# Kernel optimization log

Hardware: AMD Instinct MI355X
Metric: run time of the kernel (lower is better)

The kernel has to match this reference:

```python
import jax, jax.numpy as jnp
import numpy as np
from jax import lax

NEG = jnp.float32(-1e9)
POS = jnp.float32(1e9)


def _edt_sq(mask):
    """Exact squared Euclidean distance transform of a 2D boolean mask.

    mask: [H, W] bool, True = foreground (nonzero in scipy terms).
    Returns [H, W] float32 squared distance to nearest background (False) pixel.
    Felzenszwalb-Huttenlocher separable formulation:
      pass 1 (axis 0): 1D distance to nearest zero per column (O(H) via scans)
      pass 2 (axis 1): min-plus convolution with quadratic per row.
    """
    H, W = mask.shape
    zero = ~mask
    idx = jnp.broadcast_to(jnp.arange(H, dtype=jnp.float32)[:, None], (H, W))
    # index of last background pixel at-or-above, and next at-or-below, per column
    last0 = lax.associative_scan(jnp.maximum, jnp.where(zero, idx, NEG), axis=0)
    next0 = jnp.flip(
        lax.associative_scan(jnp.minimum, jnp.flip(jnp.where(zero, idx, POS), 0), axis=0), 0)
    d1 = jnp.minimum(idx - last0, next0 - idx)  # 1D distance along axis 0
    f = jnp.where(mask, d1 * d1, jnp.float32(0.0))  # squared axis-0 distance
    # pass 2: D[i, j] = min_j' f[i, j'] + (j - j')^2
    jq = jnp.arange(W, dtype=jnp.float32)
    q = (jq[:, None] - jq[None, :]) ** 2  # [W, W]
    def row_min(frow):  # frow: [W]
        return jnp.min(frow[None, :] + q, axis=1)  # [W]
    return lax.map(row_min, f)  # [H, W]


def setup_inputs() -> dict:
    key = jax.random.key(0)
    img = jax.random.uniform(key, (2048, 2048), dtype=jnp.float32)
    return {"img": img}


def reference(img) -> jnp.ndarray:
    mask = img > 0.5  # scipy: nonzero pixels are foreground
    d = jnp.sqrt(_edt_sq(mask))
    m = jnp.max(d)
    d = jnp.where(m > 0, d / m * 255.0, d)  # `if img.max() != 0: img = img/max*255`
    return d.astype(jnp.uint8)  # img.astype(np.uint8)
```

## Files before the change

### kernel.cpp

```cpp
#include <hip/hip_runtime.h>
#include <math.h>

typedef unsigned long long u64;

#define H 2048
#define W 2048
#define NWR 64
#define TILE 128
#define HALO 32
#define LW 192
#define LSTRIDE 193
#define DCLAMP 2900
#define NTHR 256

__device__ __attribute__((noinline)) int vfar_up(const unsigned* rmask, int col, int r, int ks) {
    for (int kk = ks - 2; kk >= 0; --kk) {
        unsigned w = rmask[kk * W + col];
        if (w) return r - (kk * 32 + (31 - __clz(w)));
    }
    return DCLAMP;
}
__device__ __attribute__((noinline)) int vfar_dn(const unsigned* rmask, int col, int r, int ks) {
    for (int kk = ks + 2; kk < NWR; ++kk) {
        unsigned w = rmask[kk * W + col];
        if (w) return (kk * 32 + (__ffs(w) - 1)) - r;
    }
    return DCLAMP;
}

__device__ __attribute__((noinline)) float f_from_mask(const unsigned* rmask, int col, int r) {
    int kw = r >> 5, b = r & 31;
    unsigned wm1 = (kw > 0)       ? rmask[(kw - 1) * W + col] : 0u;
    unsigned w0  =                  rmask[kw * W + col];
    unsigned wp1 = (kw < NWR - 1) ? rmask[(kw + 1) * W + col] : 0u;
    if ((w0 >> b) & 1u) return 0.0f;
    u64 A  = (u64)wm1 | ((u64)w0 << 32);
    u64 Bv = (u64)w0  | ((u64)wp1 << 32);
    int p = 32 + b;
    u64 Am = A & ((1ull << p) - 1ull);
    int da = Am ? (p - (63 - __clzll(Am))) : vfar_up(rmask, col, r, kw);
    u64 Bm = Bv >> (b + 1);
    int db = Bm ? __ffsll(Bm) : vfar_dn(rmask, col, r, kw);
    int d1 = min(min(da, db), DCLAMP);
    return (float)d1 * (float)d1;
}

__global__ void k1_pack(const float* __restrict__ img, unsigned* __restrict__ rmask,
                        unsigned int* __restrict__ maxp) {
    int gid = blockIdx.x * NTHR + threadIdx.x;
    if (gid == 0) *maxp = 0u;
    int col = gid & (W - 1);
    int kw  = gid >> 11;
    unsigned w = 0;
#pragma unroll
    for (int i = 0; i < 32; ++i)
        w |= (img[(size_t)(kw * 32 + i) * W + col] <= 0.5f ? 1u : 0u) << i;
    rmask[kw * W + col] = w;
}

__global__ void __launch_bounds__(NTHR)
k2_edt(const unsigned* __restrict__ rmask, float* __restrict__ dist,
       unsigned int* __restrict__ maxp) {
    __shared__ float ftile[32][LSTRIDE];
    __shared__ float smax[4];
    const int tid = threadIdx.x;
    const int c0 = blockIdx.x * TILE;
    const int ks = blockIdx.y;
    const int rbase = ks * 32;

    if (tid < LW) {
        int gc = c0 - HALO + tid;
        if (gc >= 0 && gc < W) {
            unsigned wm1 = (ks > 0)       ? rmask[(ks - 1) * W + gc] : 0u;
            unsigned w0  =                  rmask[ks * W + gc];
            unsigned wp1 = (ks < NWR - 1) ? rmask[(ks + 1) * W + gc] : 0u;
            u64 A  = (u64)wm1 | ((u64)w0 << 32);
            u64 Bv = (u64)w0  | ((u64)wp1 << 32);
#pragma unroll
            for (int i = 0; i < 32; ++i) {
                int p = 32 + i;
                u64 Am = A & ((1ull << p) - 1ull);
                int da = Am ? (p - (63 - __clzll(Am))) : vfar_up(rmask, gc, rbase + i, ks);
                u64 Bm = Bv >> (i + 1);
                int db = Bm ? __ffsll(Bm) : vfar_dn(rmask, gc, rbase + i, ks);
                int d1 = min(min(da, db), DCLAMP);
                float fd = (float)d1;
                ftile[i][tid] = ((w0 >> i) & 1u) ? 0.0f : fd * fd;
            }
        } else {
#pragma unroll
            for (int i = 0; i < 32; ++i)
                ftile[i][tid] = 1e9f;
        }
    }
    __syncthreads();

    const int i  = tid & 31;
    const int p  = tid >> 5;
    const int lc = HALO + p * 16;
    float reg[32];
#pragma unroll
    for (int k = 0; k < 32; ++k)
        reg[k] = ftile[i][lc - 8 + k];

    float res[16];
    float lmax = 0.0f;
#pragma unroll
    for (int m = 0; m < 16; ++m) {
        float best = reg[m + 8];
#pragma unroll
        for (int d = 1; d <= 8; ++d) {
            float q = (float)(d * d);
            best = fminf(best, reg[m + 8 - d] + q);
            best = fminf(best, reg[m + 8 + d] + q);
        }
        if (__builtin_expect(81.0f < best, 0)) {
            for (int d = 9; d <= HALO && (float)(d * d) < best; ++d) {
                float q = (float)(d * d);
                best = fminf(best, ftile[i][lc + m - d] + q);
                best = fminf(best, ftile[i][lc + m + d] + q);
            }
            if ((float)((HALO + 1) * (HALO + 1)) < best) {
                int r = rbase + i, jj = c0 + p * 16 + m;
                for (int d = HALO + 1; d < W && (float)(d * d) < best; ++d) {
                    float q = (float)(d * d);
                    int jm = jj - d, jp = jj + d;
                    if (jm >= 0) best = fminf(best, f_from_mask(rmask, jm, r) + q);
                    if (jp < W)  best = fminf(best, f_from_mask(rmask, jp, r) + q);
                }
            }
        }
        float rr = sqrtf(best);
        res[m] = rr;
        lmax = fmaxf(lmax, rr);
    }

    __syncthreads();
#pragma unroll
    for (int m = 0; m < 16; ++m)
        ftile[i][p * 16 + m] = res[m];
    __syncthreads();
#pragma unroll
    for (int q = 0; q < 4; ++q) {
        int r  = (tid >> 5) + 8 * q;
        int c4 = (tid & 31) * 4;
        float4 v = make_float4(ftile[r][c4], ftile[r][c4 + 1],
                               ftile[r][c4 + 2], ftile[r][c4 + 3]);
        *(float4*)(dist + (size_t)(rbase + r) * W + c0 + c4) = v;
    }

    for (int o = 32; o > 0; o >>= 1) lmax = fmaxf(lmax, __shfl_down(lmax, o, 64));
    if ((tid & 63) == 0) smax[tid >> 6] = lmax;
    __syncthreads();
    if (tid == 0)
        atomicMax(maxp, __float_as_uint(fmaxf(fmaxf(smax[0], smax[1]),
                                              fmaxf(smax[2], smax[3]))));
}

__global__ void k3_norm(int* __restrict__ out, const unsigned int* __restrict__ maxp) {
    size_t idx = ((size_t)blockIdx.x * NTHR + threadIdx.x) * 4;
    float m = __uint_as_float(*maxp);
    float4 dv = *(const float4*)((const float*)out + idx);
    float r[4] = {dv.x, dv.y, dv.z, dv.w};
    int o[4];
#pragma unroll
    for (int k = 0; k < 4; ++k) {
        float v = (m > 0.0f) ? (r[k] / m * 255.0f) : r[k];
        v = fminf(fmaxf(v, 0.0f), 255.0f);
        o[k] = (int)v;
    }
    *(int4*)(out + idx) = make_int4(o[0], o[1], o[2], o[3]);
}

extern "C" void kernel_launch(void* const* d_in, const int* in_sizes, int n_in,
                              void* d_out, int out_size, void* d_ws, size_t ws_size,
                              hipStream_t stream) {
    const float* img = (const float*)d_in[0];
    int* out = (int*)d_out;

    unsigned* rmask = (unsigned*)d_ws;
    unsigned int* maxp = (unsigned int*)((char*)d_ws + (size_t)NWR * W * 4);

    k1_pack<<<dim3(NWR * W / NTHR), dim3(NTHR), 0, stream>>>(img, rmask, maxp);
    k2_edt <<<dim3(W / TILE, NWR), dim3(NTHR), 0, stream>>>(rmask, (float*)out, maxp);
    k3_norm<<<dim3(H * W / (NTHR * 4)), dim3(NTHR), 0, stream>>>(out, maxp);
}
```

Before: 91.07 us.

## Fuse normalization into EDT kernel via grid-wide barrier on global max

Merges the normalization kernel into the EDT kernel. Each block publishes its local max, then spins on a global arrival counter until all 1024 blocks arrive, and writes the normalized int output straight from shared memory. This removes the float intermediate write and re-read plus one kernel launch. It depends on all 1024 blocks being co-resident (16 per CU on 64 CUs; launch_bounds 5), otherwise it deadlocks. It also changes the division to a multiply by a reciprocal.

```diff
diff --git a/kernel.cpp b/kernel.cpp
--- a/kernel.cpp
+++ b/kernel.cpp
@@ -12,6 +12,7 @@
 #define LSTRIDE 193
 #define DCLAMP 2900
 #define NTHR 256
+#define NBLK2 1024
 
 __device__ __attribute__((noinline)) int vfar_up(const unsigned* rmask, int col, int r, int ks) {
     for (int kk = ks - 2; kk >= 0; --kk) {
@@ -46,9 +47,9 @@
 }
 
 __global__ void k1_pack(const float* __restrict__ img, unsigned* __restrict__ rmask,
-                        unsigned int* __restrict__ maxp) {
+                        unsigned int* __restrict__ maxp, unsigned int* __restrict__ done) {
     int gid = blockIdx.x * NTHR + threadIdx.x;
-    if (gid == 0) *maxp = 0u;
+    if (gid == 0) { *maxp = 0u; *done = 0u; }
     int col = gid & (W - 1);
     int kw  = gid >> 11;
     unsigned w = 0;
@@ -58,11 +59,11 @@
     rmask[kw * W + col] = w;
 }
 
-__global__ void __launch_bounds__(NTHR)
-k2_edt(const unsigned* __restrict__ rmask, float* __restrict__ dist,
-       unsigned int* __restrict__ maxp) {
+__global__ void __launch_bounds__(NTHR, 5)
+k2_fused(const unsigned* __restrict__ rmask, int* __restrict__ out,
+         unsigned int* __restrict__ maxp, unsigned int* __restrict__ done) {
     __shared__ float ftile[32][LSTRIDE];
-    __shared__ float smax[4];
+    __shared__ float smax[5];
     const int tid = threadIdx.x;
     const int c0 = blockIdx.x * TILE;
     const int ks = blockIdx.y;
@@ -139,37 +140,38 @@
 #pragma unroll
     for (int m = 0; m < 16; ++m)
         ftile[i][p * 16 + m] = res[m];
+
+    for (int o = 32; o > 0; o >>= 1) lmax = fmaxf(lmax, __shfl_down(lmax, o, 64));
+    if ((tid & 63) == 0) smax[1 + (tid >> 6)] = lmax;
     __syncthreads();
+
+    if (tid == 0) {
+        float bm = fmaxf(fmaxf(smax[1], smax[2]), fmaxf(smax[3], smax[4]));
+        atomicMax(maxp, __float_as_uint(bm));
+        __hip_atomic_fetch_add(done, 1u, __ATOMIC_ACQ_REL, __HIP_MEMORY_SCOPE_AGENT);
+        while (__hip_atomic_load(done, __ATOMIC_ACQUIRE, __HIP_MEMORY_SCOPE_AGENT) < NBLK2)
+            __builtin_amdgcn_s_sleep(8);
+        smax[0] = __uint_as_float(__hip_atomic_load(maxp, __ATOMIC_ACQUIRE,
+                                                    __HIP_MEMORY_SCOPE_AGENT));
+    }
+    __syncthreads();
+
+    float m = smax[0];
+    float scale = (m > 0.0f) ? 1.0f / m : 0.0f;
 #pragma unroll
     for (int q = 0; q < 4; ++q) {
         int r  = (tid >> 5) + 8 * q;
         int c4 = (tid & 31) * 4;
-        float4 v = make_float4(ftile[r][c4], ftile[r][c4 + 1],
-                               ftile[r][c4 + 2], ftile[r][c4 + 3]);
-        *(float4*)(dist + (size_t)(rbase + r) * W + c0 + c4) = v;
+        int o[4];
+#pragma unroll
+        for (int k = 0; k < 4; ++k) {
+            float dv = ftile[r][c4 + k];
+            float v = (m > 0.0f) ? (dv * scale * 255.0f) : dv;
+            v = fminf(fmaxf(v, 0.0f), 255.0f);
+            o[k] = (int)v;
+        }
+        *(int4*)(out + (size_t)(rbase + r) * W + c0 + c4) = make_int4(o[0], o[1], o[2], o[3]);
     }
-
-    for (int o = 32; o > 0; o >>= 1) lmax = fmaxf(lmax, __shfl_down(lmax, o, 64));
-    if ((tid & 63) == 0) smax[tid >> 6] = lmax;
-    __syncthreads();
-    if (tid == 0)
-        atomicMax(maxp, __float_as_uint(fmaxf(fmaxf(smax[0], smax[1]),
-                                              fmaxf(smax[2], smax[3]))));
-}
-
-__global__ void k3_norm(int* __restrict__ out, const unsigned int* __restrict__ maxp) {
-    size_t idx = ((size_t)blockIdx.x * NTHR + threadIdx.x) * 4;
-    float m = __uint_as_float(*maxp);
-    float4 dv = *(const float4*)((const float*)out + idx);
-    float r[4] = {dv.x, dv.y, dv.z, dv.w};
-    int o[4];
-#pragma unroll
-    for (int k = 0; k < 4; ++k) {
-        float v = (m > 0.0f) ? (r[k] / m * 255.0f) : r[k];
-        v = fminf(fmaxf(v, 0.0f), 255.0f);
-        o[k] = (int)v;
-    }
-    *(int4*)(out + idx) = make_int4(o[0], o[1], o[2], o[3]);
 }
 
 extern "C" void kernel_launch(void* const* d_in, const int* in_sizes, int n_in,
@@ -180,8 +182,8 @@
 
     unsigned* rmask = (unsigned*)d_ws;
     unsigned int* maxp = (unsigned int*)((char*)d_ws + (size_t)NWR * W * 4);
+    unsigned int* done = maxp + 1;
 
-    k1_pack<<<dim3(NWR * W / NTHR), dim3(NTHR), 0, stream>>>(img, rmask, maxp);
-    k2_edt <<<dim3(W / TILE, NWR), dim3(NTHR), 0, stream>>>(rmask, (float*)out, maxp);
-    k3_norm<<<dim3(H * W / (NTHR * 4)), dim3(NTHR), 0, stream>>>(out, maxp);
+    k1_pack <<<dim3(NWR * W / NTHR), dim3(NTHR), 0, stream>>>(img, rmask, maxp, done);
+    k2_fused<<<dim3(W / TILE, NWR), dim3(NTHR), 0, stream>>>(rmask, out, maxp, done);
 }
```

Result: slower. 134.7 us (+48.0%).
